# Performance work log

Measured on AMD Instinct MI355X. Metric: run time of the kernel, lower is better.

The kernel has to match this reference:

```python
import jax, jax.numpy as jnp
import numpy as np

R = 12          # resolution (H = W = G); L = R**3 = 1728
HEADS = 12


def setup_inputs() -> dict:
    key = jax.random.key(0)
    k1, k2, k3 = jax.random.split(key, 3)
    B, L, C = 4, R ** 3, 768
    qkv = jax.random.normal(k1, (3, B, L, C), dtype=jnp.float32)
    lepe_w = jax.random.normal(k2, (C, 1, 3, 3, 3), dtype=jnp.float32) * 0.05
    lepe_b = jax.random.normal(k3, (C,), dtype=jnp.float32) * 0.01
    return {"qkv": qkv, "lepe_w": lepe_w, "lepe_b": lepe_b}


def reference(qkv, lepe_w, lepe_b):
    # qkv: [3, B, L, C]; idx=0 => window == full volume, so attention is dense over L.
    q, k, v = qkv[0], qkv[1], qkv[2]
    B, L, C = q.shape
    hd = C // HEADS
    scale = hd ** -0.5

    # im2cswin with full-volume window preserves token order: [B, L, C] -> [B, H, L, d]
    qh = q.reshape(B, L, HEADS, hd).transpose(0, 2, 1, 3)
    kh = k.reshape(B, L, HEADS, hd).transpose(0, 2, 1, 3)

    # get_lepe: v -> [B, C, R, R, R], depthwise 3x3x3 conv (groups=C)
    v_img = v.transpose(0, 2, 1).reshape(B, C, R, R, R)
    lepe = jax.lax.conv_general_dilated(
        v_img, lepe_w, window_strides=(1, 1, 1), padding="SAME",
        dimension_numbers=("NCDHW", "OIDHW", "NCDHW"), feature_group_count=C,
    ) + lepe_b[None, :, None, None, None]
    lepe = lepe.reshape(B, HEADS, hd, L).transpose(0, 1, 3, 2)   # [B, H, L, d]
    vh = v_img.reshape(B, HEADS, hd, L).transpose(0, 1, 3, 2)    # [B, H, L, d]

    attn = jax.nn.softmax(jnp.einsum("bhqd,bhkd->bhqk", qh * scale, kh), axis=-1)
    out = jnp.einsum("bhqk,bhkd->bhqd", attn, vh) + lepe          # [B, H, L, d]

    # windows2img with full window is an inverse reshape back to [B, L, C]
    return out.transpose(0, 2, 1, 3).reshape(B, L, C)
```

## Files before the change

### kernel.cpp

```cpp
#include <hip/hip_runtime.h>

#define RR 12
#define LL 1728
#define CC 768
#define HEADS 12
#define HD 64
#define BATCH 4

typedef __attribute__((ext_vector_type(8))) short bf8;
typedef __attribute__((ext_vector_type(4))) float f4;

__device__ inline unsigned short f2bf(float x) {
  unsigned int u = __float_as_uint(x);
  return (unsigned short)((u + 0x7FFFu + ((u >> 16) & 1u)) >> 16);
}
__device__ inline unsigned short f2bfr(float x) {
  return (unsigned short)((__float_as_uint(x) + 0x8000u) >> 16);
}

__device__ inline float fast_exp2(float x) {
#if __has_builtin(__builtin_amdgcn_exp2f)
  return __builtin_amdgcn_exp2f(x);
#else
  return exp2f(x);
#endif
}

__device__ inline void gld16(const unsigned short* g, unsigned short* l) {
  __builtin_amdgcn_global_load_lds((const __attribute__((address_space(1))) unsigned int*)g,
                                   (__attribute__((address_space(3))) unsigned int*)l, 16, 0, 0);
}

#define QSCALE 0.1803368801111244f

#define NLEPE 5184
#define NPREP 1296

__global__ __launch_bounds__(256) void combined_kernel(const float* __restrict__ qkv,
                                                       const float* __restrict__ w,
                                                       const float* __restrict__ bias,
                                                       unsigned short* __restrict__ qb,
                                                       unsigned short* __restrict__ kb,
                                                       unsigned short* __restrict__ vT,
                                                       float* __restrict__ out) {
  __shared__ __align__(16) unsigned char smem[27648];
  const int bid = blockIdx.x;
  const int t = threadIdx.x;

  if (bid < NLEPE) {
    const int xg = (bid % 3) * 4;
    const int line = (bid / 3) % 144;
    const int ct = (bid / 432) % 3;
    const int b = bid / 1296;
    const int z = line / RR;
    const int y = line % RR;
    const int c0 = ct * 256;
    const int c = c0 + t;
    float* w_lds = (float*)smem;

    {
      const float* wsrc = w + (size_t)c0 * 27;
#pragma unroll
      for (int i = 0; i < 7; ++i) {
        const int idx = i * 256 + t;
        if (idx < 1728) *(float4*)&w_lds[idx * 4] = *(const float4*)&wsrc[idx * 4];
      }
    }
    __syncthreads();
    float wreg[27];
#pragma unroll
    for (int j = 0; j < 27; ++j) wreg[j] = w_lds[t * 27 + j];

    const float* vb = qkv + ((size_t)(2 * BATCH + b)) * LL * CC + c;
    const float bv = bias[c];
    float acc[4] = {bv, bv, bv, bv};

#pragma unroll
    for (int dz = -1; dz <= 1; ++dz) {
#pragma unroll
      for (int dy = -1; dy <= 1; ++dy) {
        const int zz = z + dz, yy = y + dy;
        const bool lineok = ((unsigned)zz < RR) & ((unsigned)yy < RR);
        const int base = (zz * RR + yy) * RR;
        float v6[6];
#pragma unroll
        for (int p = 0; p < 6; ++p) {
          const int xx = xg - 1 + p;
          const bool ok = lineok & ((unsigned)xx < RR);
          const int lp = ok ? base + xx : 0;
          const float vv = vb[(size_t)lp * CC];
          v6[p] = ok ? vv : 0.f;
        }
        const int jb = ((dz + 1) * 3 + (dy + 1)) * 3;
        const float wL = wreg[jb], wC = wreg[jb + 1], wR = wreg[jb + 2];
#pragma unroll
        for (int i = 0; i < 4; ++i)
          acc[i] += wL * v6[i] + wC * v6[i + 1] + wR * v6[i + 2];
      }
    }
    const size_t obase = ((size_t)b * LL + line * RR + xg) * CC + c;
#pragma unroll
    for (int i = 0; i < 4; ++i) out[obase + (size_t)i * CC] = acc[i];

  } else {
    const int p = bid - NLEPE;
    const int lt = p % 27;
    const int h = (p / 27) % HEADS;
    const int b = p / (27 * HEADS);
    unsigned short* tl = (unsigned short*)smem;

    {
      const int r0 = t >> 4;
      const int c4 = (t & 15) * 4;
#pragma unroll
      for (int pi = 0; pi < 4; ++pi) {
        const int row = lt * 64 + pi * 16 + r0;
        const size_t off = ((size_t)b * LL + row) * CC + h * HD + c4;
        const float4 qv = *(const float4*)(qkv + off);
        ushort4 oq;
        oq.x = f2bf(qv.x * QSCALE); oq.y = f2bf(qv.y * QSCALE);
        oq.z = f2bf(qv.z * QSCALE); oq.w = f2bf(qv.w * QSCALE);
        *(ushort4*)(qb + off) = oq;
        const float4 kv = *(const float4*)(qkv + (size_t)BATCH * LL * CC + off);
        ushort4 ok;
        ok.x = f2bf(kv.x); ok.y = f2bf(kv.y); ok.z = f2bf(kv.z); ok.w = f2bf(kv.w);
        *(ushort4*)(kb + off) = ok;
      }
    }

    const float* vsrc = qkv + ((size_t)(2 * BATCH + b)) * LL * CC;
#pragma unroll
    for (int it = 0; it < 4; ++it) {
      const int idx = it * 256 + t;
      const int lrow = idx >> 4;
      const int c4 = (idx & 15) * 4;
      const float4 vv = *(const float4*)(vsrc + (size_t)(lt * 64 + lrow) * CC + h * HD + c4);
      tl[(c4 + 0) * 65 + lrow] = f2bf(vv.x);
      tl[(c4 + 1) * 65 + lrow] = f2bf(vv.y);
      tl[(c4 + 2) * 65 + lrow] = f2bf(vv.z);
      tl[(c4 + 3) * 65 + lrow] = f2bf(vv.w);
    }
    __syncthreads();
#pragma unroll
    for (int it = 0; it < 4; ++it) {
      const int idx = it * 256 + t;
      const int drow = idx >> 4;
      const int u = idx & 15;
      const int s4 = u * 4;
      const int kbase = (((u >> 3) * 2 + (u & 1)) << 4) + (((u >> 1) & 3) << 2);
      ushort4 o;
      o.x = tl[drow * 65 + kbase + 0];
      o.y = tl[drow * 65 + kbase + 1];
      o.z = tl[drow * 65 + kbase + 2];
      o.w = tl[drow * 65 + kbase + 3];
      *(ushort4*)(vT + (((size_t)(b * HEADS + h) * HD + drow) * LL) + lt * 64 + s4) = o;
    }
  }
}

__global__ __launch_bounds__(256) void attn_kernel(const unsigned short* __restrict__ qb,
                                                   const unsigned short* __restrict__ kb,
                                                   const unsigned short* __restrict__ vT,
                                                   float* __restrict__ out) {
  __shared__ unsigned short k_lds[3][64 * 64];
  __shared__ unsigned short v_lds[3][64 * 64];

  const int g = blockIdx.x;
  const int xcd = g & 7;
  const int ix = g >> 3;
  const int qt = ix % 14;
  const int bh = xcd * 6 + ix / 14;
  const int h = bh % HEADS;
  const int b = bh / HEADS;

  const int t = threadIdx.x;
  const int lane = t & 63;
  const int wave = t >> 6;
  const int m = lane & 15;
  const int quad = lane >> 4;

  bf8 qf[2][2];
#pragma unroll
  for (int sub = 0; sub < 2; ++sub) {
    int row = qt * 128 + sub * 64 + wave * 16 + m;
    row = row < LL ? row : LL - 1;
    const size_t qbase = ((size_t)(b * LL + row)) * CC + h * HD;
    qf[sub][0] = *(const bf8*)(qb + qbase + quad * 8);
    qf[sub][1] = *(const bf8*)(qb + qbase + 32 + quad * 8);
  }

  int koff[2], voff[2], ldsb[2];
#pragma unroll
  for (int j = 0; j < 2; ++j) {
    const int cidx = (j * 4 + wave) * 64 + lane;
    const int row = cidx >> 3;
    const int sc = (cidx & 7) ^ (row & 7);
    koff[j] = row * CC + sc * 8;
    voff[j] = row * LL + sc * 8;
    ldsb[j] = (j * 4 + wave) * 512;
  }

  const unsigned short* kgb = kb + (size_t)b * LL * CC + h * HD;
  const unsigned short* vgb = vT + ((size_t)(b * HEADS + h) * HD) * LL;

#define ISSUE_TILE(KT, BUF)                                                             \
  {                                                                                     \
    const size_t ko = (size_t)(KT) * 64 * CC;                                           \
    const int vo = (KT) * 64;                                                           \
    gld16(kgb + ko + koff[0], &k_lds[BUF][ldsb[0]]);                                    \
    gld16(kgb + ko + koff[1], &k_lds[BUF][ldsb[1]]);                                    \
    gld16(vgb + vo + voff[0], &v_lds[BUF][ldsb[0]]);                                    \
    gld16(vgb + vo + voff[1], &v_lds[BUF][ldsb[1]]);                                    \
  }

  ISSUE_TILE(0, 0)
  ISSUE_TILE(1, 1)

  f4 o_acc[2][4] = {};
  float psum[2] = {0.f, 0.f};

#define ATTN_BODY(KT, CUR, WAITN, DOISSUE)                                              \
  {                                                                                     \
    __asm__ volatile("s_waitcnt vmcnt(" #WAITN ")" ::: "memory");                       \
    __builtin_amdgcn_s_barrier();                                                       \
    if (DOISSUE) ISSUE_TILE((KT) + 2, ((CUR) + 2) % 3)                                  \
    f4 s_acc[2][4] = {};                                                                \
    __builtin_amdgcn_s_setprio(1);                                                      \
    _Pragma("unroll")                                                                   \
    for (int nt = 0; nt < 4; ++nt) {                                                    \
      _Pragma("unroll")                                                                 \
      for (int ks = 0; ks < 2; ++ks) {                                                  \
        const int cc = ((ks * 4 + quad) ^ (m & 7)) * 8;                                 \
        const bf8 kf = *(const bf8*)&k_lds[CUR][(nt * 16 + m) * 64 + cc];               \
        s_acc[0][nt] = __builtin_amdgcn_mfma_f32_16x16x32_bf16(kf, qf[0][ks], s_acc[0][nt], 0, 0, 0); \
        s_acc[1][nt] = __builtin_amdgcn_mfma_f32_16x16x32_bf16(kf, qf[1][ks], s_acc[1][nt], 0, 0, 0); \
      }                                                                                 \
    }                                                                                   \
    __builtin_amdgcn_s_setprio(0);                                                      \
    bf8 pf[2][2];                                                                       \
    _Pragma("unroll")                                                                   \
    for (int sub = 0; sub < 2; ++sub) {                                                 \
      _Pragma("unroll")                                                                 \
      for (int ks = 0; ks < 2; ++ks) {                                                  \
        union { bf8 v; unsigned int w[4]; } pu;                                         \
        _Pragma("unroll")                                                               \
        for (int bb = 0; bb < 2; ++bb) {                                                \
          const int nt = ks * 2 + bb;                                                   \
          const float p0 = fast_exp2(s_acc[sub][nt][0]);                                \
          const float p1 = fast_exp2(s_acc[sub][nt][1]);                                \
          const float p2 = fast_exp2(s_acc[sub][nt][2]);                                \
          const float p3 = fast_exp2(s_acc[sub][nt][3]);                                \
          psum[sub] += (p0 + p1) + (p2 + p3);                                           \
          pu.w[bb * 2 + 0] = (unsigned int)f2bfr(p0) | ((unsigned int)f2bfr(p1) << 16); \
          pu.w[bb * 2 + 1] = (unsigned int)f2bfr(p2) | ((unsigned int)f2bfr(p3) << 16); \
        }                                                                               \
        pf[sub][ks] = pu.v;                                                             \
      }                                                                                 \
    }                                                                                   \
    __builtin_amdgcn_s_setprio(1);                                                      \
    _Pragma("unroll")                                                                   \
    for (int nt = 0; nt < 4; ++nt) {                                                    \
      _Pragma("unroll")                                                                 \
      for (int ks = 0; ks < 2; ++ks) {                                                  \
        const int cc = ((ks * 4 + quad) ^ (m & 7)) * 8;                                 \
        const bf8 vf = *(const bf8*)&v_lds[CUR][(nt * 16 + m) * 64 + cc];               \
        o_acc[0][nt] = __builtin_amdgcn_mfma_f32_16x16x32_bf16(vf, pf[0][ks], o_acc[0][nt], 0, 0, 0); \
        o_acc[1][nt] = __builtin_amdgcn_mfma_f32_16x16x32_bf16(vf, pf[1][ks], o_acc[1][nt], 0, 0, 0); \
      }                                                                                 \
    }                                                                                   \
    __builtin_amdgcn_s_setprio(0);                                                      \
  }

  for (int i = 0; i < 8; ++i) {
    const int t0 = i * 3;
    ATTN_BODY(t0 + 0, 0, 4, true)
    ATTN_BODY(t0 + 1, 1, 4, true)
    ATTN_BODY(t0 + 2, 2, 4, true)
  }
  ATTN_BODY(24, 0, 4, true)
  ATTN_BODY(25, 1, 4, false)
  ATTN_BODY(26, 2, 0, false)
#undef ATTN_BODY
#undef ISSUE_TILE

#pragma unroll
  for (int sub = 0; sub < 2; ++sub) {
    float s = psum[sub];
    s += __shfl_xor(s, 16);
    s += __shfl_xor(s, 32);
    const float inv = 1.0f / s;
    const int rowq = qt * 128 + sub * 64 + wave * 16 + m;
    if (rowq < LL) {
      float* op = out + ((size_t)b * LL + rowq) * CC + h * HD + quad * 4;
#pragma unroll
      for (int nt = 0; nt < 4; ++nt) {
        float4 o4 = *(float4*)&op[nt * 16];
        o4.x += o_acc[sub][nt][0] * inv;
        o4.y += o_acc[sub][nt][1] * inv;
        o4.z += o_acc[sub][nt][2] * inv;
        o4.w += o_acc[sub][nt][3] * inv;
        *(float4*)&op[nt * 16] = o4;
      }
    }
  }
}

extern "C" void kernel_launch(void* const* d_in, const int* in_sizes, int n_in,
                              void* d_out, int out_size, void* d_ws, size_t ws_size,
                              hipStream_t stream) {
  (void)in_sizes; (void)n_in; (void)ws_size; (void)out_size;
  const float* qkv = (const float*)d_in[0];
  const float* lepe_w = (const float*)d_in[1];
  const float* lepe_b = (const float*)d_in[2];
  float* out = (float*)d_out;

  const size_t NE = (size_t)BATCH * LL * CC;
  unsigned short* qb = (unsigned short*)d_ws;
  unsigned short* kb = qb + NE;
  unsigned short* vT = kb + NE;

  combined_kernel<<<dim3(NLEPE + NPREP), 256, 0, stream>>>(qkv, lepe_w, lepe_b, qb, kb, vT, out);
  attn_kernel<<<dim3(672), 256, 0, stream>>>(qb, kb, vT, out);
}
```

Measured before the change: 189.5 us.

## Use 512-thread attention blocks with 256-query tiles and staggered KV start

Each attention block now runs 8 waves over 256 query rows, so every K/V tile loaded into shared memory serves twice as many queries and the grid halves to 336 blocks. Each thread issues one K and one V global-to-LDS load per tile instead of two, and the wait count drops to match. Blocks start their KV sweep at a tile offset chosen by query tile, so blocks of the same head read different K/V tiles at the same moment. In exchange there are fewer blocks to fill the CUs, barriers span more waves, and the launch-bounds hint asks for four blocks per CU.

```diff
diff --git a/kernel.cpp b/kernel.cpp
--- a/kernel.cpp
+++ b/kernel.cpp
@@ -158,20 +158,21 @@
   }
 }
 
-__global__ __launch_bounds__(256) void attn_kernel(const unsigned short* __restrict__ qb,
-                                                   const unsigned short* __restrict__ kb,
-                                                   const unsigned short* __restrict__ vT,
-                                                   float* __restrict__ out) {
+__global__ __launch_bounds__(512, 4) void attn_kernel(const unsigned short* __restrict__ qb,
+                                                      const unsigned short* __restrict__ kb,
+                                                      const unsigned short* __restrict__ vT,
+                                                      float* __restrict__ out) {
   __shared__ unsigned short k_lds[3][64 * 64];
   __shared__ unsigned short v_lds[3][64 * 64];
 
   const int g = blockIdx.x;
   const int xcd = g & 7;
   const int ix = g >> 3;
-  const int qt = ix % 14;
-  const int bh = xcd * 6 + ix / 14;
+  const int qt = ix % 7;
+  const int bh = xcd * 6 + ix / 7;
   const int h = bh % HEADS;
   const int b = bh / HEADS;
+  const int stg = (qt * 4) % 27;
 
   const int t = threadIdx.x;
   const int lane = t & 63;
@@ -182,22 +183,21 @@
   bf8 qf[2][2];
 #pragma unroll
   for (int sub = 0; sub < 2; ++sub) {
-    int row = qt * 128 + sub * 64 + wave * 16 + m;
+    int row = qt * 256 + sub * 128 + wave * 16 + m;
     row = row < LL ? row : LL - 1;
     const size_t qbase = ((size_t)(b * LL + row)) * CC + h * HD;
     qf[sub][0] = *(const bf8*)(qb + qbase + quad * 8);
     qf[sub][1] = *(const bf8*)(qb + qbase + 32 + quad * 8);
   }
 
-  int koff[2], voff[2], ldsb[2];
-#pragma unroll
-  for (int j = 0; j < 2; ++j) {
-    const int cidx = (j * 4 + wave) * 64 + lane;
+  int koff, voff, ldsb;
+  {
+    const int cidx = wave * 64 + lane;
     const int row = cidx >> 3;
     const int sc = (cidx & 7) ^ (row & 7);
-    koff[j] = row * CC + sc * 8;
-    voff[j] = row * LL + sc * 8;
-    ldsb[j] = (j * 4 + wave) * 512;
+    koff = row * CC + sc * 8;
+    voff = row * LL + sc * 8;
+    ldsb = wave * 512;
   }
 
   const unsigned short* kgb = kb + (size_t)b * LL * CC + h * HD;
@@ -205,25 +205,27 @@
 
 #define ISSUE_TILE(KT, BUF)                                                             \
   {                                                                                     \
-    const size_t ko = (size_t)(KT) * 64 * CC;                                           \
-    const int vo = (KT) * 64;                                                           \
-    gld16(kgb + ko + koff[0], &k_lds[BUF][ldsb[0]]);                                    \
-    gld16(kgb + ko + koff[1], &k_lds[BUF][ldsb[1]]);                                    \
-    gld16(vgb + vo + voff[0], &v_lds[BUF][ldsb[0]]);                                    \
-    gld16(vgb + vo + voff[1], &v_lds[BUF][ldsb[1]]);                                    \
-  }
-
-  ISSUE_TILE(0, 0)
-  ISSUE_TILE(1, 1)
+    gld16(kgb + (size_t)(KT) * (64 * CC) + koff, &k_lds[BUF][ldsb]);                    \
+    gld16(vgb + (KT) * 64 + voff, &v_lds[BUF][ldsb]);                                   \
+  }
+
+  ISSUE_TILE(stg, 0)
+  {
+    int k1 = stg + 1; if (k1 >= 27) k1 -= 27;
+    ISSUE_TILE(k1, 1)
+  }
 
   f4 o_acc[2][4] = {};
   float psum[2] = {0.f, 0.f};
 
-#define ATTN_BODY(KT, CUR, WAITN, DOISSUE)                                              \
+#define ATTN_BODY(I, STG, WAITN, DOISSUE)                                               \
   {                                                                                     \
     __asm__ volatile("s_waitcnt vmcnt(" #WAITN ")" ::: "memory");                       \
     __builtin_amdgcn_s_barrier();                                                       \
-    if (DOISSUE) ISSUE_TILE((KT) + 2, ((CUR) + 2) % 3)                                  \
+    if (DOISSUE) {                                                                      \
+      int ktn = stg + (I) + 2; if (ktn >= 27) ktn -= 27;                                \
+      ISSUE_TILE(ktn, ((STG) + 2) % 3)                                                  \
+    }                                                                                   \
     f4 s_acc[2][4] = {};                                                                \
     __builtin_amdgcn_s_setprio(1);                                                      \
     _Pragma("unroll")                                                                   \
@@ -231,7 +233,7 @@
       _Pragma("unroll")                                                                 \
       for (int ks = 0; ks < 2; ++ks) {                                                  \
         const int cc = ((ks * 4 + quad) ^ (m & 7)) * 8;                                 \
-        const bf8 kf = *(const bf8*)&k_lds[CUR][(nt * 16 + m) * 64 + cc];               \
+        const bf8 kf = *(const bf8*)&k_lds[STG][(nt * 16 + m) * 64 + cc];               \
         s_acc[0][nt] = __builtin_amdgcn_mfma_f32_16x16x32_bf16(kf, qf[0][ks], s_acc[0][nt], 0, 0, 0); \
         s_acc[1][nt] = __builtin_amdgcn_mfma_f32_16x16x32_bf16(kf, qf[1][ks], s_acc[1][nt], 0, 0, 0); \
       }                                                                                 \
@@ -263,7 +265,7 @@
       _Pragma("unroll")                                                                 \
       for (int ks = 0; ks < 2; ++ks) {                                                  \
         const int cc = ((ks * 4 + quad) ^ (m & 7)) * 8;                                 \
-        const bf8 vf = *(const bf8*)&v_lds[CUR][(nt * 16 + m) * 64 + cc];               \
+        const bf8 vf = *(const bf8*)&v_lds[STG][(nt * 16 + m) * 64 + cc];               \
         o_acc[0][nt] = __builtin_amdgcn_mfma_f32_16x16x32_bf16(vf, pf[0][ks], o_acc[0][nt], 0, 0, 0); \
         o_acc[1][nt] = __builtin_amdgcn_mfma_f32_16x16x32_bf16(vf, pf[1][ks], o_acc[1][nt], 0, 0, 0); \
       }                                                                                 \
@@ -271,14 +273,14 @@
     __builtin_amdgcn_s_setprio(0);                                                      \
   }
 
-  for (int i = 0; i < 8; ++i) {
-    const int t0 = i * 3;
-    ATTN_BODY(t0 + 0, 0, 4, true)
-    ATTN_BODY(t0 + 1, 1, 4, true)
-    ATTN_BODY(t0 + 2, 2, 4, true)
-  }
-  ATTN_BODY(24, 0, 4, true)
-  ATTN_BODY(25, 1, 4, false)
+  for (int ip = 0; ip < 8; ++ip) {
+    const int i0 = ip * 3;
+    ATTN_BODY(i0 + 0, 0, 2, true)
+    ATTN_BODY(i0 + 1, 1, 2, true)
+    ATTN_BODY(i0 + 2, 2, 2, true)
+  }
+  ATTN_BODY(24, 0, 2, true)
+  ATTN_BODY(25, 1, 2, false)
   ATTN_BODY(26, 2, 0, false)
 #undef ATTN_BODY
 #undef ISSUE_TILE
@@ -289,7 +291,7 @@
     s += __shfl_xor(s, 16);
     s += __shfl_xor(s, 32);
     const float inv = 1.0f / s;
-    const int rowq = qt * 128 + sub * 64 + wave * 16 + m;
+    const int rowq = qt * 256 + sub * 128 + wave * 16 + m;
     if (rowq < LL) {
       float* op = out + ((size_t)b * LL + rowq) * CC + h * HD + quad * 4;
 #pragma unroll
@@ -320,5 +322,5 @@
   unsigned short* vT = kb + NE;
 
   combined_kernel<<<dim3(NLEPE + NPREP), 256, 0, stream>>>(qkv, lepe_w, lepe_b, qb, kb, vT, out);
-  attn_kernel<<<dim3(672), 256, 0, stream>>>(qb, kb, vT, out);
-}
+  attn_kernel<<<dim3(336), 512, 0, stream>>>(qb, kb, vT, out);
+}
```

Result: no change. 191.3 us (+0.9%).
